# Kernel optimization log

Hardware: AMD Instinct MI355X
Metric: run time of the kernel (lower is better)

## Reference

```python
import jax, jax.numpy as jnp
import numpy as np

N_NODES = 50000
N_EDGES = 800000
IN_CH = 128
HID = 32
HEADS = 4
OUT_CH = 16
NEG_SLOPE = 0.2  # PyG GATConv default LeakyReLU slope


def setup_inputs() -> dict:
    key = jax.random.key(0)
    ks = jax.random.split(key, 12)
    x = jax.random.normal(ks[0], (N_NODES, IN_CH), dtype=jnp.float32)
    edge_index = jax.random.randint(ks[1], (2, N_EDGES), 0, N_NODES, dtype=jnp.int32)
    edge_attr = jax.random.uniform(ks[2], (N_EDGES,), dtype=jnp.float32)
    s = 0.1
    W1 = jax.random.normal(ks[3], (IN_CH, HEADS * HID), dtype=jnp.float32) * s
    a_src1 = jax.random.normal(ks[4], (HEADS, HID), dtype=jnp.float32) * s
    a_dst1 = jax.random.normal(ks[5], (HEADS, HID), dtype=jnp.float32) * s
    b1 = jnp.zeros((HEADS * HID,), dtype=jnp.float32)
    W2 = jax.random.normal(ks[6], (HEADS * HID, OUT_CH), dtype=jnp.float32) * s
    a_src2 = jax.random.normal(ks[7], (1, OUT_CH), dtype=jnp.float32) * s
    a_dst2 = jax.random.normal(ks[8], (1, OUT_CH), dtype=jnp.float32) * s
    b2 = jnp.zeros((OUT_CH,), dtype=jnp.float32)
    return {"x": x, "edge_index": edge_index, "edge_attr": edge_attr,
            "W1": W1, "a_src1": a_src1, "a_dst1": a_dst1, "b1": b1,
            "W2": W2, "a_src2": a_src2, "a_dst2": a_dst2, "b2": b2}


def gat_conv(x, src, dst, num_nodes, W, a_src, a_dst, bias, concat):
    H, C = a_src.shape
    h = (x @ W).reshape(-1, H, C)              # [N,H,C]
    al_src = jnp.sum(h * a_src, axis=-1)       # [N,H]
    al_dst = jnp.sum(h * a_dst, axis=-1)       # [N,H]
    e = jax.nn.leaky_relu(al_src[src] + al_dst[dst], NEG_SLOPE)  # [E,H]
    # segment softmax over incoming edges of each destination node
    m = jax.ops.segment_max(e, dst, num_segments=num_nodes)
    ex = jnp.exp(e - m[dst])
    denom = jax.ops.segment_sum(ex, dst, num_segments=num_nodes)
    alpha = ex / (denom[dst] + 1e-16)          # [E,H]
    out = jax.ops.segment_sum(h[src] * alpha[..., None], dst, num_segments=num_nodes)  # [N,H,C]
    out = out.reshape(num_nodes, H * C) if concat else out.mean(axis=1)
    return out + bias


def reference(x, edge_index, edge_attr, W1, a_src1, a_dst1, b1, W2, a_src2, a_dst2, b2):
    # edge_attr is ignored by GATConv when edge_dim is None (PyG default)
    N = x.shape[0]
    loop = jnp.arange(N, dtype=edge_index.dtype)  # PyG add_self_loops=True
    src = jnp.concatenate([edge_index[0], loop])
    dst = jnp.concatenate([edge_index[1], loop])
    h = jax.nn.elu(gat_conv(x, src, dst, N, W1, a_src1, a_dst1, b1, True))
    out = gat_conv(h, src, dst, N, W2, a_src2, a_dst2, b2, False)
    return jax.nn.log_softmax(out, axis=1)
```

## Files before the change

### kernel.cpp

```cpp
#include <hip/hip_runtime.h>

#define N_NODESC 50000
#define E0C      800000
#define E_TOTC   850000
#define IN_CHC   128
#define HCC      128
#define HEADSC   4
#define OUT_CHC  16
#define NEG_SLOPE 0.2f
#define G1_ROWS  32
#define NBUCK    196
#define BNODES   256
#define SBLK     128
#define CHUNK    6656

__device__ __forceinline__ float lrelu(float v){ return v > 0.f ? v : NEG_SLOPE * v; }

__device__ __forceinline__ unsigned int f2bf(float f){
  unsigned int b = __float_as_uint(f);
  return (b + 0x7fffu + ((b >> 16) & 1u)) >> 16;
}
__device__ __forceinline__ float bf2f(unsigned int lo16){
  return __uint_as_float(lo16 << 16);
}
__device__ __forceinline__ int xswz(int r, int k){ return r ^ (((k >> 4) & 7) << 2); }

__global__ void __launch_bounds__(512) k_gemm1(const float* __restrict__ x, const float* __restrict__ W1,
        const float* __restrict__ a_s, const float* __restrict__ a_d,
        unsigned int* __restrict__ h1b, float* __restrict__ al_s, float* __restrict__ al_d)
{
  __shared__ __align__(16) unsigned int Wl[IN_CHC*HCC/2];
  __shared__ __align__(16) float xT[IN_CHC][G1_ROWS];
  int tid = threadIdx.x;
  for (int i = tid; i < IN_CHC*HCC/2; i += 512){
    float2 w = *(const float2*)&W1[(size_t)i*2];
    Wl[i] = f2bf(w.x) | (f2bf(w.y) << 16);
  }
  int row0 = blockIdx.x * G1_ROWS;
  {
    int r  = tid >> 4;
    int kc = (tid & 15) * 8;
    int rr = row0 + r; if (rr > N_NODESC-1) rr = N_NODESC-1;
    const float* xp = &x[(size_t)rr*IN_CHC + kc];
    int sc = xswz(r, kc);
    #pragma unroll
    for (int j = 0; j < 8; j += 4){
      float4 v = *(const float4*)&xp[j];
      xT[kc+j+0][sc] = v.x;
      xT[kc+j+1][sc] = v.y;
      xT[kc+j+2][sc] = v.z;
      xT[kc+j+3][sc] = v.w;
    }
  }
  __syncthreads();
  int wave = tid >> 6, lane = tid & 63;
  int c0 = lane * 2;
  int rbase = wave * 4;
  float acc[4][2];
  #pragma unroll
  for (int j = 0; j < 4; j++){ acc[j][0] = 0.f; acc[j][1] = 0.f; }
  #pragma unroll 4
  for (int k = 0; k < IN_CHC; k++){
    unsigned int uw = Wl[k*64 + lane];
    float wx = __uint_as_float(uw << 16);
    float wy = __uint_as_float(uw & 0xFFFF0000u);
    float4 xa = *(const float4*)&xT[k][xswz(rbase, k)];
    acc[0][0] = fmaf(xa.x, wx, acc[0][0]); acc[0][1] = fmaf(xa.x, wy, acc[0][1]);
    acc[1][0] = fmaf(xa.y, wx, acc[1][0]); acc[1][1] = fmaf(xa.y, wy, acc[1][1]);
    acc[2][0] = fmaf(xa.z, wx, acc[2][0]); acc[2][1] = fmaf(xa.z, wy, acc[2][1]);
    acc[3][0] = fmaf(xa.w, wx, acc[3][0]); acc[3][1] = fmaf(xa.w, wy, acc[3][1]);
  }
  float as0 = a_s[c0], as1 = a_s[c0+1];
  float ad0 = a_d[c0], ad1 = a_d[c0+1];
  #pragma unroll
  for (int j = 0; j < 4; j++){
    int row = row0 + rbase + j;
    if (row >= N_NODESC) break;
    h1b[(size_t)row*64 + lane] = f2bf(acc[j][0]) | (f2bf(acc[j][1]) << 16);
    float ps = acc[j][0]*as0 + acc[j][1]*as1;
    float pd = acc[j][0]*ad0 + acc[j][1]*ad1;
    #pragma unroll
    for (int m = 1; m < 16; m <<= 1){ ps += __shfl_xor(ps, m, 64); pd += __shfl_xor(pd, m, 64); }
    if ((lane & 15) == 0){
      al_s[row*HEADSC + (lane>>4)] = ps;
      al_d[row*HEADSC + (lane>>4)] = pd;
    }
  }
}

__global__ void __launch_bounds__(256) k_binA(const int* __restrict__ ei, int* __restrict__ bh){
  __shared__ int h[NBUCK];
  int tid = threadIdx.x, b = blockIdx.x;
  for (int i = tid; i < NBUCK; i += 256) h[i] = 0;
  __syncthreads();
  int e0 = b*CHUNK, e1 = e0 + CHUNK; if (e1 > E_TOTC) e1 = E_TOTC;
  for (int e = e0 + tid; e < e1; e += 256){
    int d = (e < E0C) ? ei[E0C + e] : (e - E0C);
    atomicAdd(&h[d >> 8], 1);
  }
  __syncthreads();
  for (int i = tid; i < NBUCK; i += 256) bh[b*NBUCK + i] = h[i];
}

__global__ void __launch_bounds__(256) k_binscan(int* __restrict__ bh, int* __restrict__ bstart){
  __shared__ int buf[256];
  int tid = threadIdx.x;
  int tot = 0;
  if (tid < NBUCK)
    for (int b = 0; b < SBLK; b++) tot += bh[b*NBUCK + tid];
  buf[tid] = (tid < NBUCK) ? tot : 0;
  __syncthreads();
  #pragma unroll
  for (int off = 1; off < 256; off <<= 1){
    int t = (tid >= off) ? buf[tid - off] : 0;
    __syncthreads();
    buf[tid] += t; __syncthreads();
  }
  int excl = buf[tid] - ((tid < NBUCK) ? tot : 0);
  if (tid < NBUCK) bstart[tid] = excl;
  if (tid == 0) bstart[NBUCK] = E_TOTC;
  __syncthreads();
  if (tid < NBUCK){
    int run = excl;
    for (int b = 0; b < SBLK; b++){
      int t = bh[b*NBUCK + tid];
      bh[b*NBUCK + tid] = run;
      run += t;
    }
  }
}

__global__ void __launch_bounds__(256) k_binB(const int* __restrict__ ei, const int* __restrict__ bh,
                                              unsigned int* __restrict__ binbuf){
  __shared__ int h[NBUCK];
  int tid = threadIdx.x, b = blockIdx.x;
  for (int i = tid; i < NBUCK; i += 256) h[i] = bh[b*NBUCK + i];
  __syncthreads();
  int e0 = b*CHUNK, e1 = e0 + CHUNK; if (e1 > E_TOTC) e1 = E_TOTC;
  for (int e = e0 + tid; e < e1; e += 256){
    int s, d;
    if (e < E0C){ d = ei[E0C + e]; s = ei[e]; }
    else { s = e - E0C; d = s; }
    int pos = atomicAdd(&h[d >> 8], 1);
    binbuf[pos] = ((unsigned int)d << 16) | (unsigned int)s;
  }
}

__global__ void __launch_bounds__(256) k_binC(const unsigned int* __restrict__ binbuf,
                                              const int* __restrict__ bstart,
                                              int* __restrict__ rp, int* __restrict__ srcs){
  __shared__ int lcnt[BNODES];
  __shared__ int buf[BNODES];
  __shared__ int pfx[BNODES];
  int tid = threadIdx.x, k = blockIdx.x;
  int lo = k * BNODES;
  int b0 = bstart[k], b1 = bstart[k+1];
  lcnt[tid] = 0;
  __syncthreads();
  for (int i = b0 + tid; i < b1; i += 256){
    int d = binbuf[i] >> 16;
    atomicAdd(&lcnt[d - lo], 1);
  }
  __syncthreads();
  int v = lcnt[tid];
  buf[tid] = v;
  __syncthreads();
  #pragma unroll
  for (int off = 1; off < 256; off <<= 1){
    int t = (tid >= off) ? buf[tid - off] : 0;
    __syncthreads();
    buf[tid] += t; __syncthreads();
  }
  int excl = buf[tid] - v;
  pfx[tid] = excl;
  int node = lo + tid;
  if (node < N_NODESC) rp[node] = b0 + excl;
  if (k == 0 && tid == 0) rp[N_NODESC] = E_TOTC;
  lcnt[tid] = 0;
  __syncthreads();
  for (int i = b0 + tid; i < b1; i += 256){
    unsigned int u = binbuf[i];
    int d = u >> 16;
    int r = atomicAdd(&lcnt[d - lo], 1);
    srcs[b0 + pfx[d - lo] + r] = (int)(u & 0xffffu);
  }
}

__global__ void __launch_bounds__(256) k_node1(const unsigned int* __restrict__ h1b,
        const float* __restrict__ al_s, const float* __restrict__ al_d,
        const int* __restrict__ rp, const int* __restrict__ srcs,
        const float* __restrict__ b1, float* __restrict__ hout)
{
  int wave = threadIdx.x >> 6, lane = threadIdx.x & 63;
  int n = blockIdx.x*4 + wave;
  if (n >= N_NODESC) return;
  int beg = rp[n], end = rp[n+1];
  int h = lane >> 4;
  float adh = al_d[n*4 + h];
  float dsum = 0.f, acc0 = 0.f, acc1 = 0.f;
  #pragma unroll 4
  for (int p = beg; p < end; p++){
    int s = srcs[p];
    float a = __expf(lrelu(al_s[s*4 + h] + adh));
    unsigned int u = h1b[(size_t)s*64 + lane];
    dsum += a;
    acc0 = fmaf(a, bf2f(u & 0xffffu), acc0);
    acc1 = fmaf(a, bf2f(u >> 16), acc1);
  }
  float inv = 1.f / (dsum + 1e-16f);
  int c0 = lane*2;
  float o0 = acc0*inv + b1[c0], o1 = acc1*inv + b1[c0+1];
  o0 = o0 > 0.f ? o0 : __expf(o0) - 1.f;
  o1 = o1 > 0.f ? o1 : __expf(o1) - 1.f;
  *(float2*)&hout[(size_t)n*HCC + c0] = make_float2(o0, o1);
}

__global__ void __launch_bounds__(256) k_gemm2(const float* __restrict__ hin, const float* __restrict__ W2,
        const float* __restrict__ a_s, const float* __restrict__ a_d,
        unsigned int* __restrict__ h2b, float* __restrict__ al_s, float* __restrict__ al_d)
{
  __shared__ __align__(16) float Wl[IN_CHC*OUT_CHC];
  __shared__ __align__(16) float xr[4][4][IN_CHC];
  int tid = threadIdx.x;
  for (int i = tid*4; i < IN_CHC*OUT_CHC; i += 256*4)
    *(float4*)&Wl[i] = *(const float4*)&W2[i];
  __syncthreads();
  int wave = tid >> 6, lane = tid & 63;
  int r = lane >> 4, c = lane & 15;
  int row0 = blockIdx.x*16 + wave*4;
  for (int rr = 0; rr < 4; rr++){
    float2 v = *(const float2*)&hin[(size_t)(row0+rr)*IN_CHC + lane*2];
    *(float2*)&xr[wave][rr][lane*2] = v;
  }
  float acc = 0.f;
  #pragma unroll 8
  for (int k = 0; k < IN_CHC; k++)
    acc = fmaf(xr[wave][r][k], Wl[k*OUT_CHC + c], acc);
  int row = row0 + r;
  float other = __shfl_xor(acc, 1, 64);
  if ((c & 1) == 0)
    h2b[(size_t)row*8 + (c >> 1)] = f2bf(acc) | (f2bf(other) << 16);
  float ps = acc * a_s[c];
  float pd = acc * a_d[c];
  #pragma unroll
  for (int m = 1; m < 16; m <<= 1){ ps += __shfl_xor(ps, m, 64); pd += __shfl_xor(pd, m, 64); }
  if (c == 0){ al_s[row] = ps; al_d[row] = pd; }
}

__global__ void __launch_bounds__(256) k_node2(const unsigned int* __restrict__ h2b,
        const float* __restrict__ al_s, const float* __restrict__ al_d,
        const int* __restrict__ rp, const int* __restrict__ srcs,
        const float* __restrict__ b2, float* __restrict__ out)
{
  int wave = threadIdx.x >> 6, lane = threadIdx.x & 63;
  int n = blockIdx.x*4 + wave;
  if (n >= N_NODESC) return;
  int beg = rp[n], end = rp[n+1];
  float ad = al_d[n];
  int c = lane & 15, jg = lane >> 4;
  unsigned int hi = (c & 1);
  int widx = c >> 1;
  float dsum = 0.f, acc = 0.f;
  #pragma unroll 4
  for (int p = beg + jg; p < end; p += 4){
    int s = srcs[p];
    float a = __expf(lrelu(al_s[s] + ad));
    unsigned int u = h2b[(size_t)s*8 + widx];
    float hv = __uint_as_float(hi ? (u & 0xFFFF0000u) : (u << 16));
    dsum += a;
    acc = fmaf(a, hv, acc);
  }
  dsum += __shfl_xor(dsum, 16, 64);
  dsum += __shfl_xor(dsum, 32, 64);
  acc += __shfl_xor(acc, 16, 64);
  acc += __shfl_xor(acc, 32, 64);
  float inv = 1.f / (dsum + 1e-16f);
  float v = acc*inv + b2[c];
  float mm = v;
  #pragma unroll
  for (int o = 1; o < 16; o <<= 1) mm = fmaxf(mm, __shfl_xor(mm, o, 64));
  float se = __expf(v - mm);
  #pragma unroll
  for (int o = 1; o < 16; o <<= 1) se += __shfl_xor(se, o, 64);
  if (jg == 0) out[n*OUT_CHC + c] = v - mm - __logf(se);
}

extern "C" void kernel_launch(void* const* d_in, const int* in_sizes, int n_in,
                              void* d_out, int out_size, void* d_ws, size_t ws_size,
                              hipStream_t stream)
{
  const float* x   = (const float*)d_in[0];
  const int*   ei  = (const int*)d_in[1];
  const float* W1  = (const float*)d_in[3];
  const float* as1 = (const float*)d_in[4];
  const float* ad1 = (const float*)d_in[5];
  const float* b1  = (const float*)d_in[6];
  const float* W2  = (const float*)d_in[7];
  const float* as2 = (const float*)d_in[8];
  const float* ad2 = (const float*)d_in[9];
  const float* b2  = (const float*)d_in[10];
  float* out = (float*)d_out;

  char* ws = (char*)d_ws;
  size_t off = 0;
  auto alloc = [&](size_t bytes)->void*{
    void* p = ws + off;
    off = (off + bytes + 255) & ~(size_t)255;
    return p;
  };
  unsigned int* h1b = (unsigned int*)alloc((size_t)N_NODESC*64*4);
  float* hout  = (float*)alloc((size_t)N_NODESC*HCC*4);
  float* al_s1 = (float*)alloc((size_t)N_NODESC*HEADSC*4);
  float* al_d1 = (float*)alloc((size_t)N_NODESC*HEADSC*4);
  unsigned int* h2b = (unsigned int*)alloc((size_t)N_NODESC*8*4);
  float* al_s2 = (float*)alloc((size_t)N_NODESC*4);
  float* al_d2 = (float*)alloc((size_t)N_NODESC*4);
  int* rp      = (int*)alloc((size_t)(N_NODESC+1)*4);
  int* srcs    = (int*)alloc((size_t)E_TOTC*4);
  int* bh      = (int*)alloc((size_t)SBLK*NBUCK*4);
  int* bstart  = (int*)alloc((size_t)(NBUCK+1)*4);
  unsigned int* binbuf = (unsigned int*)alloc((size_t)E_TOTC*4);

  k_gemm1<<<(N_NODESC+G1_ROWS-1)/G1_ROWS, 512, 0, stream>>>(x, W1, as1, ad1, h1b, al_s1, al_d1);
  k_binA<<<SBLK, 256, 0, stream>>>(ei, bh);
  k_binscan<<<1, 256, 0, stream>>>(bh, bstart);
  k_binB<<<SBLK, 256, 0, stream>>>(ei, bh, binbuf);
  k_binC<<<NBUCK, 256, 0, stream>>>(binbuf, bstart, rp, srcs);
  k_node1<<<(N_NODESC+3)/4, 256, 0, stream>>>(h1b, al_s1, al_d1, rp, srcs, b1, hout);
  k_gemm2<<<N_NODESC/16, 256, 0, stream>>>(hout, W2, as2, ad2, h2b, al_s2, al_d2);
  k_node2<<<(N_NODESC+3)/4, 256, 0, stream>>>(h2b, al_s2, al_d2, rp, srcs, b2, out);
}
```

Baseline: 165.6 us.

## Use bf16 MFMA for first-layer GEMM with swizzled LDS tiles

Replaces the scalar FMA layer-1 projection with MFMA 16x16x32 bf16 instructions. Both x and W1 are converted to bf16 and stored in XOR-swizzled LDS layouts, and blocks now cover 64 rows with 256 threads. The attention logits are reduced from the MFMA accumulator layout with shuffles. Rounding x to bf16 adds precision loss, and each block still reloads and transposes W1 with strided global reads.

```diff
diff --git a/kernel.cpp b/kernel.cpp
--- a/kernel.cpp
+++ b/kernel.cpp
@@ -8,12 +8,15 @@
 #define HEADSC   4
 #define OUT_CHC  16
 #define NEG_SLOPE 0.2f
-#define G1_ROWS  32
+#define G1M      64
 #define NBUCK    196
 #define BNODES   256
 #define SBLK     128
 #define CHUNK    6656
 
+typedef __attribute__((ext_vector_type(8))) short bf16x8;
+typedef __attribute__((ext_vector_type(4))) float f32x4;
+
 __device__ __forceinline__ float lrelu(float v){ return v > 0.f ? v : NEG_SLOPE * v; }
 
 __device__ __forceinline__ unsigned int f2bf(float f){
@@ -23,67 +26,93 @@
 __device__ __forceinline__ float bf2f(unsigned int lo16){
   return __uint_as_float(lo16 << 16);
 }
-__device__ __forceinline__ int xswz(int r, int k){ return r ^ (((k >> 4) & 7) << 2); }
-
-__global__ void __launch_bounds__(512) k_gemm1(const float* __restrict__ x, const float* __restrict__ W1,
+
+__global__ void __launch_bounds__(256) k_gemm1(const float* __restrict__ x, const float* __restrict__ W1,
         const float* __restrict__ a_s, const float* __restrict__ a_d,
         unsigned int* __restrict__ h1b, float* __restrict__ al_s, float* __restrict__ al_d)
 {
-  __shared__ __align__(16) unsigned int Wl[IN_CHC*HCC/2];
-  __shared__ __align__(16) float xT[IN_CHC][G1_ROWS];
-  int tid = threadIdx.x;
-  for (int i = tid; i < IN_CHC*HCC/2; i += 512){
-    float2 w = *(const float2*)&W1[(size_t)i*2];
-    Wl[i] = f2bf(w.x) | (f2bf(w.y) << 16);
-  }
-  int row0 = blockIdx.x * G1_ROWS;
+  __shared__ __align__(16) unsigned short Wt[IN_CHC*HCC];
+  __shared__ __align__(16) unsigned short xt[G1M*IN_CHC];
+  int tid = threadIdx.x, lane = tid & 63, wave = tid >> 6;
+  int row0 = blockIdx.x * G1M;
+
+  for (int n0 = 0; n0 < 128; n0 += 64){
+    int n = n0 + wave*16 + (lane & 15);
+    for (int kc = 0; kc < 128; kc += 32){
+      int k = kc + (lane >> 4)*8;
+      unsigned int u[4];
+      #pragma unroll
+      for (int j = 0; j < 8; j += 2){
+        float a = W1[(size_t)(k+j)*HCC + n];
+        float b = W1[(size_t)(k+j+1)*HCC + n];
+        u[j>>1] = f2bf(a) | (f2bf(b) << 16);
+      }
+      int idx = (n*128 + k) ^ ((n & 7) << 3);
+      *(uint4*)&Wt[idx] = make_uint4(u[0],u[1],u[2],u[3]);
+    }
+  }
   {
-    int r  = tid >> 4;
-    int kc = (tid & 15) * 8;
+    int r  = tid >> 2;
+    int kc = (tid & 3) * 32;
     int rr = row0 + r; if (rr > N_NODESC-1) rr = N_NODESC-1;
     const float* xp = &x[(size_t)rr*IN_CHC + kc];
-    int sc = xswz(r, kc);
     #pragma unroll
-    for (int j = 0; j < 8; j += 4){
-      float4 v = *(const float4*)&xp[j];
-      xT[kc+j+0][sc] = v.x;
-      xT[kc+j+1][sc] = v.y;
-      xT[kc+j+2][sc] = v.z;
-      xT[kc+j+3][sc] = v.w;
-    }
-  }
-  __syncthreads();
-  int wave = tid >> 6, lane = tid & 63;
-  int c0 = lane * 2;
-  int rbase = wave * 4;
-  float acc[4][2];
-  #pragma unroll
-  for (int j = 0; j < 4; j++){ acc[j][0] = 0.f; acc[j][1] = 0.f; }
-  #pragma unroll 4
-  for (int k = 0; k < IN_CHC; k++){
-    unsigned int uw = Wl[k*64 + lane];
-    float wx = __uint_as_float(uw << 16);
-    float wy = __uint_as_float(uw & 0xFFFF0000u);
-    float4 xa = *(const float4*)&xT[k][xswz(rbase, k)];
-    acc[0][0] = fmaf(xa.x, wx, acc[0][0]); acc[0][1] = fmaf(xa.x, wy, acc[0][1]);
-    acc[1][0] = fmaf(xa.y, wx, acc[1][0]); acc[1][1] = fmaf(xa.y, wy, acc[1][1]);
-    acc[2][0] = fmaf(xa.z, wx, acc[2][0]); acc[2][1] = fmaf(xa.z, wy, acc[2][1]);
-    acc[3][0] = fmaf(xa.w, wx, acc[3][0]); acc[3][1] = fmaf(xa.w, wy, acc[3][1]);
-  }
-  float as0 = a_s[c0], as1 = a_s[c0+1];
-  float ad0 = a_d[c0], ad1 = a_d[c0+1];
-  #pragma unroll
-  for (int j = 0; j < 4; j++){
-    int row = row0 + rbase + j;
-    if (row >= N_NODESC) break;
-    h1b[(size_t)row*64 + lane] = f2bf(acc[j][0]) | (f2bf(acc[j][1]) << 16);
-    float ps = acc[j][0]*as0 + acc[j][1]*as1;
-    float pd = acc[j][0]*ad0 + acc[j][1]*ad1;
+    for (int j = 0; j < 32; j += 8){
+      unsigned int u0 = f2bf(xp[j+0]) | (f2bf(xp[j+1]) << 16);
+      unsigned int u1 = f2bf(xp[j+2]) | (f2bf(xp[j+3]) << 16);
+      unsigned int u2 = f2bf(xp[j+4]) | (f2bf(xp[j+5]) << 16);
+      unsigned int u3 = f2bf(xp[j+6]) | (f2bf(xp[j+7]) << 16);
+      int idx = (r*128 + kc + j) ^ ((r & 7) << 3);
+      *(uint4*)&xt[idx] = make_uint4(u0,u1,u2,u3);
+    }
+  }
+  __syncthreads();
+
+  int rw = wave * 16;
+  f32x4 acc[8];
+  #pragma unroll
+  for (int t = 0; t < 8; t++) acc[t] = (f32x4){0.f,0.f,0.f,0.f};
+  #pragma unroll
+  for (int kk = 0; kk < 128; kk += 32){
+    int m  = rw + (lane & 15);
+    int ks = kk + (lane >> 4)*8;
+    bf16x8 afrag = *(bf16x8*)&xt[(m*128 + ks) ^ ((m & 7) << 3)];
     #pragma unroll
-    for (int m = 1; m < 16; m <<= 1){ ps += __shfl_xor(ps, m, 64); pd += __shfl_xor(pd, m, 64); }
-    if ((lane & 15) == 0){
-      al_s[row*HEADSC + (lane>>4)] = ps;
-      al_d[row*HEADSC + (lane>>4)] = pd;
+    for (int t = 0; t < 8; t++){
+      int n = t*16 + (lane & 15);
+      bf16x8 bfrag = *(bf16x8*)&Wt[(n*128 + ks) ^ ((n & 7) << 3)];
+      acc[t] = __builtin_amdgcn_mfma_f32_16x16x32_bf16(afrag, bfrag, acc[t], 0, 0, 0);
+    }
+  }
+
+  float asv[8], adv[8];
+  #pragma unroll
+  for (int t = 0; t < 8; t++){
+    asv[t] = a_s[t*16 + (lane & 15)];
+    adv[t] = a_d[t*16 + (lane & 15)];
+  }
+  #pragma unroll
+  for (int r = 0; r < 4; r++){
+    int row = row0 + rw + (lane >> 4)*4 + r;
+    bool ok = (row < N_NODESC);
+    #pragma unroll
+    for (int t = 0; t < 8; t++){
+      float v = acc[t][r];
+      float o = __shfl_xor(v, 1, 64);
+      int c = t*16 + (lane & 15);
+      if (ok && ((c & 1) == 0))
+        h1b[(size_t)row*64 + (c >> 1)] = f2bf(v) | (f2bf(o) << 16);
+    }
+    #pragma unroll
+    for (int h = 0; h < 4; h++){
+      float ps = acc[2*h][r]*asv[2*h] + acc[2*h+1][r]*asv[2*h+1];
+      float pd = acc[2*h][r]*adv[2*h] + acc[2*h+1][r]*adv[2*h+1];
+      #pragma unroll
+      for (int m = 1; m < 16; m <<= 1){ ps += __shfl_xor(ps, m, 64); pd += __shfl_xor(pd, m, 64); }
+      if (ok && (lane & 15) == 0){
+        al_s[row*HEADSC + h] = ps;
+        al_d[row*HEADSC + h] = pd;
+      }
     }
   }
 }
@@ -321,7 +350,7 @@
   int* bstart  = (int*)alloc((size_t)(NBUCK+1)*4);
   unsigned int* binbuf = (unsigned int*)alloc((size_t)E_TOTC*4);
 
-  k_gemm1<<<(N_NODESC+G1_ROWS-1)/G1_ROWS, 512, 0, stream>>>(x, W1, as1, ad1, h1b, al_s1, al_d1);
+  k_gemm1<<<(N_NODESC+G1M-1)/G1M, 256, 0, stream>>>(x, W1, as1, ad1, h1b, al_s1, al_d1);
   k_binA<<<SBLK, 256, 0, stream>>>(ei, bh);
   k_binscan<<<1, 256, 0, stream>>>(bh, bstart);
   k_binB<<<SBLK, 256, 0, stream>>>(ei, bh, binbuf);
```

Result: faster. 150.2 us (-9.3%).
